# Kernel tuning notes

Hardware: AMD Instinct MI355X
Metric: run time of the kernel (lower is better)

The kernel has to match this reference:

```python
import jax, jax.numpy as jnp
import numpy as np
from jax import lax

GROUPS = 32
EPS = 1e-5
COMMON_STRIDE = 4


def conv3x3(x, w):
    # x: [B,C,H,W], w: [O,I,3,3], stride 1, padding 1 ('SAME'), no bias
    return lax.conv_general_dilated(x, w, (1, 1), 'SAME',
                                    dimension_numbers=('NCHW', 'OIHW', 'NCHW'))


def group_norm(x, scale, bias):
    b, c, h, w = x.shape
    xg = x.reshape(b, GROUPS, c // GROUPS, h, w)
    mean = xg.mean(axis=(2, 3, 4), keepdims=True)
    var = xg.var(axis=(2, 3, 4), keepdims=True)
    xg = (xg - mean) * lax.rsqrt(var + EPS)
    x = xg.reshape(b, c, h, w)
    return x * scale[None, :, None, None] + bias[None, :, None, None]


def head(x, w, s, bta):
    return jax.nn.relu(group_norm(conv3x3(x, w), s, bta))


def setup_inputs() -> dict:
    key = jax.random.key(0)
    ks = jax.random.split(key, 4)
    B, Cin, H, W = 2, 256, 64, 64
    Cd, K = 128, 19
    fan3 = Cin * 9
    return {
        'x': jax.random.normal(ks[0], (B, Cin, H, W), jnp.float32),
        'w_pam': jax.random.normal(ks[1], (Cd, Cin, 3, 3), jnp.float32) * np.sqrt(2.0 / fan3),
        'gn_pam_scale': jnp.ones((Cd,), jnp.float32),
        'gn_pam_bias': jnp.zeros((Cd,), jnp.float32),
        'w_cam': jax.random.normal(ks[2], (Cd, Cin, 3, 3), jnp.float32) * np.sqrt(2.0 / fan3),
        'gn_cam_scale': jnp.ones((Cd,), jnp.float32),
        'gn_cam_bias': jnp.zeros((Cd,), jnp.float32),
        'w_pred': jax.random.normal(ks[3], (K, Cd, 1, 1), jnp.float32) * np.sqrt(2.0 / Cd),
        'b_pred': jnp.zeros((K,), jnp.float32),
    }


def reference(x, w_pam, gn_pam_scale, gn_pam_bias, w_cam, gn_cam_scale, gn_cam_bias,
              w_pred, b_pred):
    pam = head(x, w_pam, gn_pam_scale, gn_pam_bias)   # [B,C,H,W]
    cam = head(x, w_cam, gn_cam_scale, gn_cam_bias)   # [B,C,H,W]
    b, c, h, w = pam.shape
    n = h * w

    # --- PAM: spatial self-attention, unscaled QK^T softmax V (Q=K=V=pam) ---
    Bm = pam.reshape(b, c, n)                                   # [B,C,N]
    pam_w = jax.nn.softmax(jnp.einsum('bci,bcj->bij', Bm, Bm), axis=-1)  # [B,N,N]
    weighted_pam = jnp.einsum('bij,bcj->bci', pam_w, Bm).reshape(b, c, h, w)
    sum_pam = pam + weighted_pam

    # --- CAM: channel self-attention over [C,C] gram matrix ---
    Am = cam.reshape(b, c, n)                                   # [B,C,N]
    cam_w = jax.nn.softmax(jnp.einsum('bcn,bdn->bcd', Am, Am), axis=-1)  # [B,C,C]
    weighted_cam = jnp.einsum('bcd,bdn->bcn', cam_w, Am).reshape(b, c, h, w)
    sum_cam = cam + weighted_cam

    # --- predictor (1x1 conv with bias) + bilinear upsample x common_stride ---
    fused = sum_pam + sum_cam
    logits = jnp.einsum('bchw,kc->bkhw', fused, w_pred[:, :, 0, 0]) + b_pred[None, :, None, None]
    out = jax.image.resize(logits, (b, logits.shape[1], h * COMMON_STRIDE, w * COMMON_STRIDE),
                           method='bilinear')  # half-pixel centers == align_corners=False
    return out
```

## Files before the change

### kernel.cpp

```cpp
#include <hip/hip_runtime.h>

#define BB 2
#define CIN 256
#define HH 64
#define WW 64
#define NPIX 4096
#define CD 128
#define CO2 256
#define KOUT 19
#define EPSV 1e-5f
#define SPAD 4356
#define KW9 2304

typedef __attribute__((ext_vector_type(8))) short bf16x8;
typedef __attribute__((ext_vector_type(4))) float f32x4;

__device__ inline unsigned short f2bf(float f) {
  unsigned u = __float_as_uint(f);
  u += 0x7fffu + ((u >> 16) & 1u);
  return (unsigned short)(u >> 16);
}
__device__ inline float bf2f(unsigned short h) {
  return __uint_as_float((unsigned)h << 16);
}
__device__ inline void f2bf_pair(float f, unsigned short& hi, unsigned short& lo) {
  hi = f2bf(f);
  const float fhi = __uint_as_float((unsigned)hi << 16);
  lo = f2bf(f - fhi);
}

__global__ __launch_bounds__(64) void zhalo_kernel(
    unsigned short* __restrict__ xThi, unsigned short* __restrict__ xTlo)
{
  const int p = blockIdx.x;
  const int b = blockIdx.y;
  int s;
  if (p < 66) s = p;
  else if (p < 132) s = 65 * 66 + (p - 66);
  else { const int q = p - 132; s = (1 + (q >> 1)) * 66 + (q & 1) * 65; }
  const size_t o = ((size_t)b * SPAD + s) * 256 + threadIdx.x * 4;
  *reinterpret_cast<uint2*>(&xThi[o]) = make_uint2(0, 0);
  *reinterpret_cast<uint2*>(&xTlo[o]) = make_uint2(0, 0);
}

__global__ __launch_bounds__(256) void xpose_kernel(
    const float* __restrict__ x, unsigned short* __restrict__ xThi,
    unsigned short* __restrict__ xTlo)
{
  const int y = blockIdx.x;
  const int cig = blockIdx.y;
  const int b = blockIdx.z;
  __shared__ float Tl[32][65];
  const int t = threadIdx.x;
  {
    const int cl = t >> 3, pg = t & 7;
    const float* src = x + ((size_t)(b * CIN + cig * 32 + cl)) * NPIX + y * 64 + pg * 8;
    const float4 v0 = *reinterpret_cast<const float4*>(src);
    const float4 v1 = *reinterpret_cast<const float4*>(src + 4);
    Tl[cl][pg * 8 + 0] = v0.x; Tl[cl][pg * 8 + 1] = v0.y;
    Tl[cl][pg * 8 + 2] = v0.z; Tl[cl][pg * 8 + 3] = v0.w;
    Tl[cl][pg * 8 + 4] = v1.x; Tl[cl][pg * 8 + 5] = v1.y;
    Tl[cl][pg * 8 + 6] = v1.z; Tl[cl][pg * 8 + 7] = v1.w;
  }
  __syncthreads();
  {
    const int sl = t >> 2, cg = t & 3;
    unsigned short hh[8], ll[8];
    #pragma unroll
    for (int i = 0; i < 8; ++i) f2bf_pair(Tl[cg * 8 + i][sl], hh[i], ll[i]);
    uint4 ph, pl;
    ph.x = (unsigned)hh[0] | ((unsigned)hh[1] << 16);
    ph.y = (unsigned)hh[2] | ((unsigned)hh[3] << 16);
    ph.z = (unsigned)hh[4] | ((unsigned)hh[5] << 16);
    ph.w = (unsigned)hh[6] | ((unsigned)hh[7] << 16);
    pl.x = (unsigned)ll[0] | ((unsigned)ll[1] << 16);
    pl.y = (unsigned)ll[2] | ((unsigned)ll[3] << 16);
    pl.z = (unsigned)ll[4] | ((unsigned)ll[5] << 16);
    pl.w = (unsigned)ll[6] | ((unsigned)ll[7] << 16);
    const size_t o = ((size_t)b * SPAD + (y + 1) * 66 + 1 + sl) * 256 + cig * 32 + cg * 8;
    *reinterpret_cast<uint4*>(&xThi[o]) = ph;
    *reinterpret_cast<uint4*>(&xTlo[o]) = pl;
  }
}

__global__ __launch_bounds__(256) void wbconv_kernel(
    const float* __restrict__ w_pam, const float* __restrict__ w_cam,
    unsigned short* __restrict__ wbhi, unsigned short* __restrict__ wblo)
{
  const int co = blockIdx.x;
  const float* wsrc = (co < CD) ? (w_pam + (size_t)co * KW9)
                                : (w_cam + (size_t)(co - CD) * KW9);
  const int t = threadIdx.x;
  #pragma unroll
  for (int i = 0; i < 9; ++i) {
    const int idx = i * 256 + t;
    const int q = idx >> 8, ci = idx & 255;
    unsigned short h, l;
    f2bf_pair(wsrc[ci * 9 + q], h, l);
    const size_t dest = ((((size_t)(co >> 4) * 9 + q) * 8 + (ci >> 5)) * 4
                        + ((ci >> 3) & 3)) * 128 + (co & 15) * 8 + (ci & 7);
    wbhi[dest] = h;
    wblo[dest] = l;
  }
}

__global__ __launch_bounds__(256) void conv_mfma_kernel(
    const unsigned short* __restrict__ xThi, const unsigned short* __restrict__ xTlo,
    const unsigned short* __restrict__ wbhi, const unsigned short* __restrict__ wblo,
    float* __restrict__ out)
{
  const int pxt = blockIdx.x;
  const int cot = blockIdx.y;
  const int b = blockIdx.z;
  const int tid = threadIdx.x;
  const int w = tid >> 6;
  const int lane = tid & 63;
  const int m = lane & 15, g = lane >> 4;
  const int p0 = pxt * 64;
  const int y = p0 >> 6;
  const int sbase = (y + 1) * 66 + 1;

  __shared__ float Obuf[4][64][68];

  const size_t xb = (size_t)b * SPAD * 256;

  f32x4 acc[4][4];
  #pragma unroll
  for (int mt = 0; mt < 4; ++mt)
    #pragma unroll
    for (int jg = 0; jg < 4; ++jg)
      #pragma unroll
      for (int r = 0; r < 4; ++r) acc[mt][jg][r] = 0.f;

  for (int q = 0; q < 9; ++q) {
    const int dq = (q / 3 - 1) * 66 + (q % 3 - 1);
    const unsigned short* xh0 = xThi + xb + (size_t)(sbase + m + dq) * 256;
    const unsigned short* xl0 = xTlo + xb + (size_t)(sbase + m + dq) * 256;
    #pragma unroll
    for (int kk2 = 0; kk2 < 2; ++kk2) {
      const int kkc = w * 2 + kk2;
      const int ko = kkc * 32 + g * 8;
      bf16x8 bh[4], bl[4];
      #pragma unroll
      for (int jg = 0; jg < 4; ++jg) {
        bh[jg] = *reinterpret_cast<const bf16x8*>(&xh0[(size_t)(jg * 16) * 256 + ko]);
        bl[jg] = *reinterpret_cast<const bf16x8*>(&xl0[(size_t)(jg * 16) * 256 + ko]);
      }
      #pragma unroll
      for (int mt = 0; mt < 4; ++mt) {
        const size_t wbase = ((((size_t)(cot * 4 + mt) * 9 + q) * 8 + kkc) * 4 + g) * 128
                             + m * 8;
        const bf16x8 ah = *reinterpret_cast<const bf16x8*>(&wbhi[wbase]);
        const bf16x8 al = *reinterpret_cast<const bf16x8*>(&wblo[wbase]);
        #pragma unroll
        for (int jg = 0; jg < 4; ++jg) {
          acc[mt][jg] = __builtin_amdgcn_mfma_f32_16x16x32_bf16(ah, bh[jg], acc[mt][jg], 0, 0, 0);
          acc[mt][jg] = __builtin_amdgcn_mfma_f32_16x16x32_bf16(ah, bl[jg], acc[mt][jg], 0, 0, 0);
          acc[mt][jg] = __builtin_amdgcn_mfma_f32_16x16x32_bf16(al, bh[jg], acc[mt][jg], 0, 0, 0);
        }
      }
    }
  }

  #pragma unroll
  for (int mt = 0; mt < 4; ++mt)
    #pragma unroll
    for (int jg = 0; jg < 4; ++jg)
      #pragma unroll
      for (int r = 0; r < 4; ++r)
        Obuf[w][mt * 16 + g * 4 + r][jg * 16 + m] = acc[mt][jg][r];
  __syncthreads();

  const int co_l = tid >> 2;
  const int pxq = (tid & 3) * 16;
  float* op = out + ((size_t)b * CO2 + cot * 64 + co_l) * NPIX + p0 + pxq;
  #pragma unroll
  for (int i = 0; i < 4; ++i) {
    float4 s;
    s.x = Obuf[0][co_l][pxq + i * 4 + 0] + Obuf[1][co_l][pxq + i * 4 + 0]
        + Obuf[2][co_l][pxq + i * 4 + 0] + Obuf[3][co_l][pxq + i * 4 + 0];
    s.y = Obuf[0][co_l][pxq + i * 4 + 1] + Obuf[1][co_l][pxq + i * 4 + 1]
        + Obuf[2][co_l][pxq + i * 4 + 1] + Obuf[3][co_l][pxq + i * 4 + 1];
    s.z = Obuf[0][co_l][pxq + i * 4 + 2] + Obuf[1][co_l][pxq + i * 4 + 2]
        + Obuf[2][co_l][pxq + i * 4 + 2] + Obuf[3][co_l][pxq + i * 4 + 2];
    s.w = Obuf[0][co_l][pxq + i * 4 + 3] + Obuf[1][co_l][pxq + i * 4 + 3]
        + Obuf[2][co_l][pxq + i * 4 + 3] + Obuf[3][co_l][pxq + i * 4 + 3];
    *reinterpret_cast<float4*>(&op[i * 4]) = s;
  }
}

__global__ __launch_bounds__(256) void gn_stats_kernel(
    const float* __restrict__ conv, float* __restrict__ meanb, float* __restrict__ rstdb)
{
  const int g = blockIdx.x;
  const float* base = conv + (size_t)g * (4 * NPIX);
  float s = 0.f, ss = 0.f;
  const float4* b4 = reinterpret_cast<const float4*>(base);
  for (int i = threadIdx.x; i < 4096; i += 256) {
    float4 v = b4[i];
    s += v.x + v.y + v.z + v.w;
    ss += v.x * v.x + v.y * v.y + v.z * v.z + v.w * v.w;
  }
  #pragma unroll
  for (int off = 32; off > 0; off >>= 1) {
    s += __shfl_down(s, off);
    ss += __shfl_down(ss, off);
  }
  __shared__ float rs[4], rss[4];
  const int lane = threadIdx.x & 63, wv = threadIdx.x >> 6;
  if (lane == 0) { rs[wv] = s; rss[wv] = ss; }
  __syncthreads();
  if (threadIdx.x == 0) {
    const float S = rs[0] + rs[1] + rs[2] + rs[3];
    const float SS = rss[0] + rss[1] + rss[2] + rss[3];
    const float inv = 1.f / 16384.f;
    const float m = S * inv;
    const float var = SS * inv - m * m;
    meanb[g] = m;
    rstdb[g] = rsqrtf(var + EPSV);
  }
}

__global__ __launch_bounds__(256) void gn_pack_kernel(
    float* __restrict__ conv, const float* __restrict__ meanb, const float* __restrict__ rstdb,
    const float* __restrict__ sc_pam, const float* __restrict__ bi_pam,
    const float* __restrict__ sc_cam, const float* __restrict__ bi_cam,
    unsigned short* __restrict__ Kf2, unsigned short* __restrict__ Vf2)
{
  const int px0 = blockIdx.x * 64;
  const int c0  = blockIdx.y * 32;
  const int b   = blockIdx.z;
  __shared__ unsigned short Tl[32][76];
  const int t = threadIdx.x;
  {
    const int cl = t >> 3, pg = t & 7;
    const int c = c0 + cl;
    const int gi = (b * 256 + c) >> 2;
    const int head = c >> 7, cc = c & 127;
    const float mean = meanb[gi], rstd = rstdb[gi];
    const float sc = head ? sc_cam[cc] : sc_pam[cc];
    const float bi = head ? bi_cam[cc] : bi_pam[cc];
    float* src = conv + ((size_t)b * CO2 + c) * NPIX + px0 + pg * 8;
    float4 v0 = *reinterpret_cast<const float4*>(src);
    float4 v1 = *reinterpret_cast<const float4*>(src + 4);
    v0.x = fmaxf((v0.x - mean) * rstd * sc + bi, 0.f);
    v0.y = fmaxf((v0.y - mean) * rstd * sc + bi, 0.f);
    v0.z = fmaxf((v0.z - mean) * rstd * sc + bi, 0.f);
    v0.w = fmaxf((v0.w - mean) * rstd * sc + bi, 0.f);
    v1.x = fmaxf((v1.x - mean) * rstd * sc + bi, 0.f);
    v1.y = fmaxf((v1.y - mean) * rstd * sc + bi, 0.f);
    v1.z = fmaxf((v1.z - mean) * rstd * sc + bi, 0.f);
    v1.w = fmaxf((v1.w - mean) * rstd * sc + bi, 0.f);
    *reinterpret_cast<float4*>(src) = v0;
    *reinterpret_cast<float4*>(src + 4) = v1;
    Tl[cl][pg * 8 + 0] = f2bf(v0.x); Tl[cl][pg * 8 + 1] = f2bf(v0.y);
    Tl[cl][pg * 8 + 2] = f2bf(v0.z); Tl[cl][pg * 8 + 3] = f2bf(v0.w);
    Tl[cl][pg * 8 + 4] = f2bf(v1.x); Tl[cl][pg * 8 + 5] = f2bf(v1.y);
    Tl[cl][pg * 8 + 6] = f2bf(v1.z); Tl[cl][pg * 8 + 7] = f2bf(v1.w);
  }
  __syncthreads();
  if (c0 < CD) {
    unsigned short* Kb = Kf2 + (size_t)b * 524288;
    unsigned short* Vb = Vf2 + (size_t)b * 524288;
    {
      const int jblk_l = t >> 6, rem = t & 63;
      const int gk = rem >> 4, mk = rem & 15;
      const int jblk = (px0 >> 4) + jblk_l;
      const int kk = c0 >> 5;
      unsigned short h[8];
      #pragma unroll
      for (int e = 0; e < 8; ++e) h[e] = Tl[gk * 8 + e][jblk_l * 16 + mk];
      uint4 packed;
      packed.x = (unsigned)h[0] | ((unsigned)h[1] << 16);
      packed.y = (unsigned)h[2] | ((unsigned)h[3] << 16);
      packed.z = (unsigned)h[4] | ((unsigned)h[5] << 16);
      packed.w = (unsigned)h[6] | ((unsigned)h[7] << 16);
      *reinterpret_cast<uint4*>(&Kb[(size_t)(jblk * 16 + kk * 4 + gk) * 128 + mk * 8]) = packed;
    }
    {
      const int ct_l = t >> 7, kt = (t >> 6) & 1, gv = (t >> 4) & 3, mv = t & 15;
      const int ct = (c0 >> 4) + ct_l;
      const int jc = px0 >> 6;
      unsigned short h[8];
      #pragma unroll
      for (int e = 0; e < 8; ++e) h[e] = Tl[ct_l * 16 + mv][kt * 32 + gv * 8 + e];
      uint4 packed;
      packed.x = (unsigned)h[0] | ((unsigned)h[1] << 16);
      packed.y = (unsigned)h[2] | ((unsigned)h[3] << 16);
      packed.z = (unsigned)h[4] | ((unsigned)h[5] << 16);
      packed.w = (unsigned)h[6] | ((unsigned)h[7] << 16);
      *reinterpret_cast<uint4*>(
          &Vb[(size_t)(((ct * 64 + jc) * 2 + kt) * 4 + gv) * 128 + mv * 8]) = packed;
    }
  }
}

__global__ __launch_bounds__(512) void pam_mfma_kernel(
    const unsigned short* __restrict__ Kf2, const unsigned short* __restrict__ Vf2,
    unsigned short* __restrict__ Opart, float* __restrict__ mpart,
    float* __restrict__ lpart)
{
  const int tile = blockIdx.x;
  const int b = blockIdx.y;
  const int kg = blockIdx.z;
  const int q0 = tile * 32;
  const int tid = threadIdx.x;
  const int w = tid >> 6;
  const int lane = tid & 63;
  const int m = lane & 15, g = lane >> 4;

  __shared__ __align__(16) unsigned short Sl[8][32 * 72];
  __shared__ unsigned short Obuf[4][32][130];
  __shared__ float mlm[8][32], mll[8][32], mst[32], ltt[32];

  const unsigned short* Kb = Kf2 + (size_t)b * 524288;
  const unsigned short* Vb = Vf2 + (size_t)b * 524288;

  bf16x8 qf[2][4];
  #pragma unroll
  for (int s = 0; s < 2; ++s)
    #pragma unroll
    for (int kk = 0; kk < 4; ++kk)
      qf[s][kk] = *reinterpret_cast<const bf16x8*>(
          &Kb[(size_t)(((q0 >> 4) + s) * 16 + kk * 4 + g) * 128 + m * 8]);

  f32x4 oacc[2][8];
  #pragma unroll
  for (int s = 0; s < 2; ++s)
    #pragma unroll
    for (int ct = 0; ct < 8; ++ct)
      #pragma unroll
      for (int r = 0; r < 4; ++r) oacc[s][ct][r] = 0.f;

  float mrow[2][4], lrow[2][4];
  #pragma unroll
  for (int s = 0; s < 2; ++s)
    #pragma unroll
    for (int r = 0; r < 4; ++r) { mrow[s][r] = -1e30f; lrow[s][r] = 0.f; }

  for (int t = kg * 32 + w * 4; t < kg * 32 + w * 4 + 4; ++t) {
    f32x4 sacc[2][4];
    #pragma unroll
    for (int s = 0; s < 2; ++s)
      #pragma unroll
      for (int jt = 0; jt < 4; ++jt)
        #pragma unroll
        for (int r = 0; r < 4; ++r) sacc[s][jt][r] = 0.f;
    #pragma unroll
    for (int jt = 0; jt < 4; ++jt) {
      #pragma unroll
      for (int kk = 0; kk < 4; ++kk) {
        const bf16x8 kf = *reinterpret_cast<const bf16x8*>(
            &Kb[(size_t)((t * 4 + jt) * 16 + kk * 4 + g) * 128 + m * 8]);
        sacc[0][jt] = __builtin_amdgcn_mfma_f32_16x16x32_bf16(qf[0][kk], kf, sacc[0][jt], 0, 0, 0);
        sacc[1][jt] = __builtin_amdgcn_mfma_f32_16x16x32_bf16(qf[1][kk], kf, sacc[1][jt], 0, 0, 0);
      }
    }
    float facq[2];
    #pragma unroll
    for (int s = 0; s < 2; ++s) {
      float fac[4];
      #pragma unroll
      for (int r = 0; r < 4; ++r) {
        float v = fmaxf(fmaxf(sacc[s][0][r], sacc[s][1][r]), fmaxf(sacc[s][2][r], sacc[s][3][r]));
        v = fmaxf(v, __shfl_xor(v, 1));
        v = fmaxf(v, __shfl_xor(v, 2));
        v = fmaxf(v, __shfl_xor(v, 4));
        v = fmaxf(v, __shfl_xor(v, 8));
        const float mn = fmaxf(mrow[s][r], v);
        fac[r] = __expf(fmaxf(mrow[s][r] - mn, -80.f));
        mrow[s][r] = mn;
      }
      #pragma unroll
      for (int r = 0; r < 4; ++r) {
        float ls = 0.f;
        #pragma unroll
        for (int jt = 0; jt < 4; ++jt) {
          const float e = __expf(sacc[s][jt][r] - mrow[s][r]);
          ls += e;
          Sl[w][(s * 16 + g * 4 + r) * 72 + jt * 16 + m] = f2bf(e);
        }
        ls += __shfl_xor(ls, 1);
        ls += __shfl_xor(ls, 2);
        ls += __shfl_xor(ls, 4);
        ls += __shfl_xor(ls, 8);
        lrow[s][r] = lrow[s][r] * fac[r] + ls;
      }
      const int sel = m & 3;
      const float fsel = (sel == 0) ? fac[0] : (sel == 1) ? fac[1] : (sel == 2) ? fac[2] : fac[3];
      facq[s] = __shfl(fsel, ((m >> 2) << 4) | sel);
    }
    #pragma unroll
    for (int s = 0; s < 2; ++s)
      #pragma unroll
      for (int ct = 0; ct < 8; ++ct)
        #pragma unroll
        for (int r = 0; r < 4; ++r) oacc[s][ct][r] *= facq[s];
    bf16x8 pf[2][2];
    #pragma unroll
    for (int s = 0; s < 2; ++s)
      #pragma unroll
      for (int kt = 0; kt < 2; ++kt)
        pf[s][kt] = *reinterpret_cast<const bf16x8*>(&Sl[w][(s * 16 + m) * 72 + kt * 32 + g * 8]);
    #pragma unroll
    for (int ct = 0; ct < 8; ++ct) {
      #pragma unroll
      for (int kt = 0; kt < 2; ++kt) {
        const bf16x8 vf = *reinterpret_cast<const bf16x8*>(
            &Vb[(size_t)(((ct * 64 + t) * 2 + kt) * 4 + g) * 128 + m * 8]);
        oacc[0][ct] = __builtin_amdgcn_mfma_f32_16x16x32_bf16(vf, pf[0][kt], oacc[0][ct], 0, 0, 0);
        oacc[1][ct] = __builtin_amdgcn_mfma_f32_16x16x32_bf16(vf, pf[1][kt], oacc[1][ct], 0, 0, 0);
      }
    }
  }

  float mq[2], lq[2];
  #pragma unroll
  for (int s = 0; s < 2; ++s) {
    const int sel = m & 3;
    const float msel_ = (sel == 0) ? mrow[s][0] : (sel == 1) ? mrow[s][1]
                       : (sel == 2) ? mrow[s][2] : mrow[s][3];
    mq[s] = __shfl(msel_, ((m >> 2) << 4) | sel);
    const float lsel_ = (sel == 0) ? lrow[s][0] : (sel == 1) ? lrow[s][1]
                       : (sel == 2) ? lrow[s][2] : lrow[s][3];
    lq[s] = __shfl(lsel_, ((m >> 2) << 4) | sel);
  }
  if (g == 0) {
    #pragma unroll
    for (int s = 0; s < 2; ++s) { mlm[w][s * 16 + m] = mq[s]; mll[w][s * 16 + m] = lq[s]; }
  }
  __syncthreads();
  float rsw[2];
  #pragma unroll
  for (int s = 0; s < 2; ++s) {
    const int row = s * 16 + m;
    float ms = mlm[0][row];
    #pragma unroll
    for (int sw = 1; sw < 8; ++sw) ms = fmaxf(ms, mlm[sw][row]);
    rsw[s] = __expf(fmaxf(mq[s] - ms, -80.f));
  }
  if (w < 4) {
    #pragma unroll
    for (int s = 0; s < 2; ++s)
      #pragma unroll
      for (int ct = 0; ct < 8; ++ct)
        #pragma unroll
        for (int r = 0; r < 4; ++r)
          Obuf[w][s * 16 + m][ct * 16 + g * 4 + r] = f2bf(oacc[s][ct][r] * rsw[s]);
  }
  if (w == 0 && g == 0) {
    #pragma unroll
    for (int s = 0; s < 2; ++s) {
      const int row = s * 16 + m;
      float ms = mlm[0][row];
      #pragma unroll
      for (int sw = 1; sw < 8; ++sw) ms = fmaxf(ms, mlm[sw][row]);
      float lt = 0.f;
      #pragma unroll
      for (int sw = 0; sw < 8; ++sw)
        lt += mll[sw][row] * __expf(fmaxf(mlm[sw][row] - ms, -80.f));
      mst[row] = ms;
      ltt[row] = lt;
    }
  }
  __syncthreads();
  if (w >= 4) {
    #pragma unroll
    for (int s = 0; s < 2; ++s)
      #pragma unroll
      for (int ct = 0; ct < 8; ++ct)
        #pragma unroll
        for (int r = 0; r < 4; ++r) {
          unsigned short* pp = &Obuf[w - 4][s * 16 + m][ct * 16 + g * 4 + r];
          *pp = f2bf(bf2f(*pp) + oacc[s][ct][r] * rsw[s]);
        }
  }
  __syncthreads();
  const size_t pbase = ((size_t)(kg * BB + b) * 128 + tile) * 32;
  unsigned short* Op = Opart + pbase * 128;
  const int c = tid >> 2;
  const int qh = (tid & 3) * 8;
  #pragma unroll
  for (int qq = 0; qq < 8; ++qq) {
    const int row = qh + qq;
    float o = 0.f;
    #pragma unroll
    for (int sw = 0; sw < 4; ++sw) o += bf2f(Obuf[sw][row][c]);
    Op[(size_t)row * 128 + c] = f2bf(o);
  }
  if (tid < 32) {
    mpart[pbase + tid] = mst[tid];
    lpart[pbase + tid] = ltt[tid];
  }
}

__global__ __launch_bounds__(256) void pam_merge_kernel(
    const float* __restrict__ conv, const unsigned short* __restrict__ Opart,
    const float* __restrict__ mpart, const float* __restrict__ lpart,
    float* __restrict__ spam)
{
  const int tile = blockIdx.x;
  const int b = blockIdx.y;
  const int tid = threadIdx.x;
  const int c = tid & 127;
  const int rg = tid >> 7;
  const size_t i0 = ((size_t)(0 * BB + b) * 128 + tile) * 32;
  const size_t i1 = ((size_t)(1 * BB + b) * 128 + tile) * 32;
  #pragma unroll
  for (int rr = 0; rr < 16; ++rr) {
    const int row = rg * 16 + rr;
    const float m0 = mpart[i0 + row], m1 = mpart[i1 + row];
    const float ms = fmaxf(m0, m1);
    const float w0 = __expf(fmaxf(m0 - ms, -80.f));
    const float w1 = __expf(fmaxf(m1 - ms, -80.f));
    const float l = lpart[i0 + row] * w0 + lpart[i1 + row] * w1;
    const float o = bf2f(Opart[(i0 + row) * 128 + c]) * w0
                  + bf2f(Opart[(i1 + row) * 128 + c]) * w1;
    const int q = tile * 32 + row;
    spam[((size_t)b * CD + c) * NPIX + q] =
        conv[((size_t)b * CO2 + c) * NPIX + q] + o / l;
  }
}

__global__ __launch_bounds__(256) void cam_gram_kernel(
    const float* __restrict__ conv, float* __restrict__ gpart)
{
  const int slice = blockIdx.x;
  const int b = blockIdx.y;
  const float* Am = conv + ((size_t)b * CO2 + CD) * NPIX;
  __shared__ float As[128][65];
  const int tid = threadIdx.x;
  const int cgrp = tid >> 4, dgrp = tid & 15;
  float acc[8][8];
  #pragma unroll
  for (int i = 0; i < 8; ++i)
    #pragma unroll
    for (int j = 0; j < 8; ++j) acc[i][j] = 0.f;
  const int nn = tid & 63, c0 = tid >> 6;
  for (int sub = 0; sub < 2; ++sub) {
    const int n0 = slice * 128 + sub * 64;
    __syncthreads();
    #pragma unroll
    for (int k = 0; k < 32; ++k)
      As[c0 + 4 * k][nn] = Am[(size_t)(c0 + 4 * k) * NPIX + n0 + nn];
    __syncthreads();
    #pragma unroll 4
    for (int n = 0; n < 64; ++n) {
      float av[8], bv[8];
      #pragma unroll
      for (int i = 0; i < 8; ++i) av[i] = As[8 * cgrp + i][n];
      #pragma unroll
      for (int j = 0; j < 8; ++j) bv[j] = As[8 * dgrp + j][n];
      #pragma unroll
      for (int i = 0; i < 8; ++i)
        #pragma unroll
        for (int j = 0; j < 8; ++j)
          acc[i][j] += av[i] * bv[j];
    }
  }
  float* gp = gpart + (((size_t)slice * BB + b) * CD + 8 * cgrp) * CD + 8 * dgrp;
  #pragma unroll
  for (int i = 0; i < 8; ++i)
    #pragma unroll
    for (int j = 0; j < 8; ++j)
      gp[i * CD + j] = acc[i][j];
}

__global__ __launch_bounds__(128) void cam_softmax_kernel(
    const float* __restrict__ gpart, float* __restrict__ camw)
{
  const int bc = blockIdx.x;
  const int b = bc >> 7, c = bc & 127;
  const int d = threadIdx.x;
  float g = 0.f;
  for (int s = 0; s < 32; ++s)
    g += gpart[(((size_t)s * BB + b) * CD + c) * CD + d];
  float m = g;
  #pragma unroll
  for (int off = 32; off > 0; off >>= 1) m = fmaxf(m, __shfl_xor(m, off));
  __shared__ float sm[2], ssum[2];
  const int lane = d & 63, wv = d >> 6;
  if (lane == 0) sm[wv] = m;
  __syncthreads();
  m = fmaxf(sm[0], sm[1]);
  const float e = __expf(g - m);
  float s = e;
  #pragma unroll
  for (int off = 32; off > 0; off >>= 1) s += __shfl_xor(s, off);
  if (lane == 0) ssum[wv] = s;
  __syncthreads();
  camw[(size_t)bc * CD + d] = e / (ssum[0] + ssum[1]);
}

__global__ __launch_bounds__(256) void cam_apply_kernel(
    const float* __restrict__ conv, const float* __restrict__ camw, float* __restrict__ scam)
{
  const int b = blockIdx.z;
  const int c0 = blockIdx.y * 4;
  const int n = blockIdx.x * 1024 + threadIdx.x;
  const float* Am = conv + ((size_t)b * CO2 + CD) * NPIX;
  const float* Wr = camw + ((size_t)b * CD + c0) * CD;
  float acc[4][4];
  #pragma unroll
  for (int i = 0; i < 4; ++i)
    #pragma unroll
    for (int k = 0; k < 4; ++k) acc[i][k] = 0.f;
  for (int d = 0; d < CD; ++d) {
    const float w0 = Wr[d], w1 = Wr[CD + d], w2 = Wr[2 * CD + d], w3 = Wr[3 * CD + d];
    #pragma unroll
    for (int k = 0; k < 4; ++k) {
      const float a = Am[(size_t)d * NPIX + n + k * 256];
      acc[0][k] += w0 * a; acc[1][k] += w1 * a;
      acc[2][k] += w2 * a; acc[3][k] += w3 * a;
    }
  }
  #pragma unroll
  for (int i = 0; i < 4; ++i)
    #pragma unroll
    for (int k = 0; k < 4; ++k)
      scam[((size_t)b * CD + c0 + i) * NPIX + n + k * 256] =
          Am[(size_t)(c0 + i) * NPIX + n + k * 256] + acc[i][k];
}

__global__ __launch_bounds__(256) void pred_part_kernel(
    const float* __restrict__ spam, const float* __restrict__ scam,
    const float* __restrict__ wpred, float* __restrict__ psum)
{
  const int p = blockIdx.x * 256 + threadIdx.x;
  const int slice = blockIdx.y;
  const int b = blockIdx.z;
  float acc[KOUT];
  #pragma unroll
  for (int k = 0; k < KOUT; ++k) acc[k] = 0.f;
  const float* sp = spam + (size_t)b * CD * NPIX + p;
  const float* sc = scam + (size_t)b * CD * NPIX + p;
  #pragma unroll
  for (int ci = 0; ci < 16; ++ci) {
    const int c = slice * 16 + ci;
    const float f = sp[(size_t)c * NPIX] + sc[(size_t)c * NPIX];
    #pragma unroll
    for (int k = 0; k < KOUT; ++k)
      acc[k] += f * wpred[k * CD + c];
  }
  #pragma unroll
  for (int k = 0; k < KOUT; ++k)
    psum[(((size_t)slice * BB + b) * KOUT + k) * NPIX + p] = acc[k];
}

__global__ __launch_bounds__(256) void pred_reduce_kernel(
    const float* __restrict__ psum, const float* __restrict__ bpred,
    float* __restrict__ logit)
{
  const int p = blockIdx.x * 256 + threadIdx.x;
  const int b = blockIdx.y;
  #pragma unroll
  for (int k = 0; k < KOUT; ++k) {
    float s = bpred[k];
    #pragma unroll
    for (int sl = 0; sl < 8; ++sl)
      s += psum[(((size_t)sl * BB + b) * KOUT + k) * NPIX + p];
    logit[((size_t)b * KOUT + k) * NPIX + p] = s;
  }
}

__global__ __launch_bounds__(256) void upsample_kernel(
    const float* __restrict__ logit, float* __restrict__ out)
{
  const int idx = blockIdx.x * 256 + threadIdx.x;
  if (idx >= BB * KOUT * 256 * 256) return;
  const int ox = idx & 255;
  const int oy = (idx >> 8) & 255;
  const int plane = idx >> 16;
  const float* src = logit + (size_t)plane * NPIX;
  const float sy = (oy + 0.5f) * 0.25f - 0.5f;
  const float sx = (ox + 0.5f) * 0.25f - 0.5f;
  const float fyf = floorf(sy), fxf = floorf(sx);
  const float wy = sy - fyf, wx = sx - fxf;
  const int y0 = (int)fyf, x0 = (int)fxf;
  const int y0c = y0 < 0 ? 0 : y0;
  const int y1c = (y0 + 1 > 63) ? 63 : y0 + 1;
  const int x0c = x0 < 0 ? 0 : x0;
  const int x1c = (x0 + 1 > 63) ? 63 : x0 + 1;
  const float v00 = src[y0c * 64 + x0c], v01 = src[y0c * 64 + x1c];
  const float v10 = src[y1c * 64 + x0c], v11 = src[y1c * 64 + x1c];
  const float top = v00 + (v01 - v00) * wx;
  const float bot = v10 + (v11 - v10) * wx;
  out[idx] = top + (bot - top) * wy;
}

extern "C" void kernel_launch(void* const* d_in, const int* in_sizes, int n_in,
                              void* d_out, int out_size, void* d_ws, size_t ws_size,
                              hipStream_t stream) {
  (void)in_sizes; (void)n_in; (void)out_size; (void)ws_size;
  const float* x      = (const float*)d_in[0];
  const float* w_pam  = (const float*)d_in[1];
  const float* s_pam  = (const float*)d_in[2];
  const float* b_pam  = (const float*)d_in[3];
  const float* w_cam  = (const float*)d_in[4];
  const float* s_cam  = (const float*)d_in[5];
  const float* b_cam  = (const float*)d_in[6];
  const float* w_pred = (const float*)d_in[7];
  const float* b_pred = (const float*)d_in[8];
  float* out_f = (float*)d_out;
  float* ws0 = (float*)d_ws;

  float* conv  = ws0;
  unsigned short* xThi = (unsigned short*)(ws0 + 2097152);
  unsigned short* xTlo = xThi + (size_t)BB * SPAD * 256;
  unsigned short* wbhi = (unsigned short*)(ws0 + 4327424);
  unsigned short* wblo = wbhi + (size_t)CO2 * KW9;
  float* gpart = ws0 + 3145728;
  unsigned short* Opart = (unsigned short*)(ws0 + 3145728);
  float* mpart = ws0 + 4194304;
  float* lpart = ws0 + 4227072;
  float* psum  = ws0 + 3145728;
  float* camw  = ws0 + 4950016;
  float* meanb = ws0 + 4982784;
  float* rstdb = ws0 + 4982912;
  float* logit = ws0 + 4983040;

  unsigned short* Kf2 = xThi;
  unsigned short* Vf2 = Kf2 + 1048576;

  float* spam = out_f;
  float* scam = out_f + 1048576;

  zhalo_kernel<<<dim3(260, 2), 64, 0, stream>>>(xThi, xTlo);
  xpose_kernel<<<dim3(64, 8, 2), 256, 0, stream>>>(x, xThi, xTlo);
  wbconv_kernel<<<256, 256, 0, stream>>>(w_pam, w_cam, wbhi, wblo);
  conv_mfma_kernel<<<dim3(64, 4, 2), 256, 0, stream>>>(xThi, xTlo, wbhi, wblo, conv);
  gn_stats_kernel<<<128, 256, 0, stream>>>(conv, meanb, rstdb);
  gn_pack_kernel<<<dim3(64, 8, 2), 256, 0, stream>>>(conv, meanb, rstdb,
      s_pam, b_pam, s_cam, b_cam, Kf2, Vf2);
  cam_gram_kernel<<<dim3(32, 2), 256, 0, stream>>>(conv, gpart);
  cam_softmax_kernel<<<256, 128, 0, stream>>>(gpart, camw);
  cam_apply_kernel<<<dim3(4, 32, 2), 256, 0, stream>>>(conv, camw, scam);
  pam_mfma_kernel<<<dim3(128, 2, 2), 512, 0, stream>>>(Kf2, Vf2, Opart, mpart, lpart);
  pam_merge_kernel<<<dim3(128, 2), 256, 0, stream>>>(conv, Opart, mpart, lpart, spam);
  pred_part_kernel<<<dim3(16, 8, 2), 256, 0, stream>>>(spam, scam, w_pred, psum);
  pred_reduce_kernel<<<dim3(16, 2), 256, 0, stream>>>(psum, b_pred, logit);
  upsample_kernel<<<9728, 256, 0, stream>>>(logit, out_f);
}
```

Measured before the change: 247.9 us.

## Compute CAM gram matrix with split-bf16 MFMA from packed fragments

The CAM channel gram matrix now runs on bf16 MFMA instructions instead of an FP32 SIMT outer-product kernel. gn_pack writes the CAM activations as hi/lo bf16 pairs in an MFMA fragment layout, and three MFMAs per tile approximate FP32 accuracy. The new gram kernel reduces over waves in shared memory and writes the final gram directly, so the softmax no longer sums 32 partial slices. The trade-off is extra pack work and hi/lo storage, and the gram launches only 16 blocks, which may leave most compute units idle.

```diff
diff --git a/kernel.cpp b/kernel.cpp
--- a/kernel.cpp
+++ b/kernel.cpp
@@ -225,12 +225,13 @@
     float* __restrict__ conv, const float* __restrict__ meanb, const float* __restrict__ rstdb,
     const float* __restrict__ sc_pam, const float* __restrict__ bi_pam,
     const float* __restrict__ sc_cam, const float* __restrict__ bi_cam,
-    unsigned short* __restrict__ Kf2, unsigned short* __restrict__ Vf2)
+    unsigned short* __restrict__ Kf2, unsigned short* __restrict__ Vf2,
+    unsigned short* __restrict__ Cfhi, unsigned short* __restrict__ Cflo)
 {
   const int px0 = blockIdx.x * 64;
   const int c0  = blockIdx.y * 32;
   const int b   = blockIdx.z;
-  __shared__ unsigned short Tl[32][76];
+  __shared__ float Tl[32][72];
   const int t = threadIdx.x;
   {
     const int cl = t >> 3, pg = t & 7;
@@ -253,10 +254,10 @@
     v1.w = fmaxf((v1.w - mean) * rstd * sc + bi, 0.f);
     *reinterpret_cast<float4*>(src) = v0;
     *reinterpret_cast<float4*>(src + 4) = v1;
-    Tl[cl][pg * 8 + 0] = f2bf(v0.x); Tl[cl][pg * 8 + 1] = f2bf(v0.y);
-    Tl[cl][pg * 8 + 2] = f2bf(v0.z); Tl[cl][pg * 8 + 3] = f2bf(v0.w);
-    Tl[cl][pg * 8 + 4] = f2bf(v1.x); Tl[cl][pg * 8 + 5] = f2bf(v1.y);
-    Tl[cl][pg * 8 + 6] = f2bf(v1.z); Tl[cl][pg * 8 + 7] = f2bf(v1.w);
+    Tl[cl][pg * 8 + 0] = v0.x; Tl[cl][pg * 8 + 1] = v0.y;
+    Tl[cl][pg * 8 + 2] = v0.z; Tl[cl][pg * 8 + 3] = v0.w;
+    Tl[cl][pg * 8 + 4] = v1.x; Tl[cl][pg * 8 + 5] = v1.y;
+    Tl[cl][pg * 8 + 6] = v1.z; Tl[cl][pg * 8 + 7] = v1.w;
   }
   __syncthreads();
   if (c0 < CD) {
@@ -269,7 +270,7 @@
       const int kk = c0 >> 5;
       unsigned short h[8];
       #pragma unroll
-      for (int e = 0; e < 8; ++e) h[e] = Tl[gk * 8 + e][jblk_l * 16 + mk];
+      for (int e = 0; e < 8; ++e) h[e] = f2bf(Tl[gk * 8 + e][jblk_l * 16 + mk]);
       uint4 packed;
       packed.x = (unsigned)h[0] | ((unsigned)h[1] << 16);
       packed.y = (unsigned)h[2] | ((unsigned)h[3] << 16);
@@ -283,7 +284,7 @@
       const int jc = px0 >> 6;
       unsigned short h[8];
       #pragma unroll
-      for (int e = 0; e < 8; ++e) h[e] = Tl[ct_l * 16 + mv][kt * 32 + gv * 8 + e];
+      for (int e = 0; e < 8; ++e) h[e] = f2bf(Tl[ct_l * 16 + mv][kt * 32 + gv * 8 + e]);
       uint4 packed;
       packed.x = (unsigned)h[0] | ((unsigned)h[1] << 16);
       packed.y = (unsigned)h[2] | ((unsigned)h[3] << 16);
@@ -292,7 +293,139 @@
       *reinterpret_cast<uint4*>(
           &Vb[(size_t)(((ct * 64 + jc) * 2 + kt) * 4 + gv) * 128 + mv * 8]) = packed;
     }
-  }
+  } else {
+    const int ct_l = t >> 7, kk_l = (t >> 6) & 1, gc = (t >> 4) & 3, mc = t & 15;
+    const int ctg = ((c0 - CD) >> 4) + ct_l;
+    const int kkg = (px0 >> 5) + kk_l;
+    unsigned short hh[8], ll[8];
+    #pragma unroll
+    for (int e = 0; e < 8; ++e)
+      f2bf_pair(Tl[ct_l * 16 + mc][kk_l * 32 + gc * 8 + e], hh[e], ll[e]);
+    uint4 ph, pl;
+    ph.x = (unsigned)hh[0] | ((unsigned)hh[1] << 16);
+    ph.y = (unsigned)hh[2] | ((unsigned)hh[3] << 16);
+    ph.z = (unsigned)hh[4] | ((unsigned)hh[5] << 16);
+    ph.w = (unsigned)hh[6] | ((unsigned)hh[7] << 16);
+    pl.x = (unsigned)ll[0] | ((unsigned)ll[1] << 16);
+    pl.y = (unsigned)ll[2] | ((unsigned)ll[3] << 16);
+    pl.z = (unsigned)ll[4] | ((unsigned)ll[5] << 16);
+    pl.w = (unsigned)ll[6] | ((unsigned)ll[7] << 16);
+    const size_t o = (((size_t)(b * 128 + kkg) * 8 + ctg) * 4 + gc) * 128 + mc * 8;
+    *reinterpret_cast<uint4*>(&Cfhi[o]) = ph;
+    *reinterpret_cast<uint4*>(&Cflo[o]) = pl;
+  }
+}
+
+__global__ __launch_bounds__(512) void cam_gram_mfma_kernel(
+    const unsigned short* __restrict__ Cfhi, const unsigned short* __restrict__ Cflo,
+    float* __restrict__ graw)
+{
+  const int dt = blockIdx.x;
+  const int b = blockIdx.y;
+  const int tid = threadIdx.x;
+  const int w = tid >> 6;
+  const int lane = tid & 63;
+  const int m = lane & 15, g = lane >> 4;
+
+  __shared__ float Gbuf[4][128][17];
+
+  f32x4 acc[8];
+  #pragma unroll
+  for (int ct = 0; ct < 8; ++ct)
+    #pragma unroll
+    for (int r = 0; r < 4; ++r) acc[ct][r] = 0.f;
+
+  for (int kk = w * 16; kk < w * 16 + 16; ++kk) {
+    const size_t base = (size_t)(b * 128 + kk) * 8;
+    const bf16x8 dh = *reinterpret_cast<const bf16x8*>(&Cfhi[((base + dt) * 4 + g) * 128 + m * 8]);
+    const bf16x8 dl = *reinterpret_cast<const bf16x8*>(&Cflo[((base + dt) * 4 + g) * 128 + m * 8]);
+    #pragma unroll
+    for (int ct = 0; ct < 8; ++ct) {
+      const bf16x8 ah = *reinterpret_cast<const bf16x8*>(&Cfhi[((base + ct) * 4 + g) * 128 + m * 8]);
+      const bf16x8 al = *reinterpret_cast<const bf16x8*>(&Cflo[((base + ct) * 4 + g) * 128 + m * 8]);
+      acc[ct] = __builtin_amdgcn_mfma_f32_16x16x32_bf16(ah, dh, acc[ct], 0, 0, 0);
+      acc[ct] = __builtin_amdgcn_mfma_f32_16x16x32_bf16(ah, dl, acc[ct], 0, 0, 0);
+      acc[ct] = __builtin_amdgcn_mfma_f32_16x16x32_bf16(al, dh, acc[ct], 0, 0, 0);
+    }
+  }
+
+  if (w < 4) {
+    #pragma unroll
+    for (int ct = 0; ct < 8; ++ct)
+      #pragma unroll
+      for (int r = 0; r < 4; ++r)
+        Gbuf[w][ct * 16 + g * 4 + r][m] = acc[ct][r];
+  }
+  __syncthreads();
+  if (w >= 4) {
+    #pragma unroll
+    for (int ct = 0; ct < 8; ++ct)
+      #pragma unroll
+      for (int r = 0; r < 4; ++r)
+        Gbuf[w - 4][ct * 16 + g * 4 + r][m] += acc[ct][r];
+  }
+  __syncthreads();
+  const int c = tid >> 2;
+  const int d0 = (tid & 3) * 4;
+  #pragma unroll
+  for (int j = 0; j < 4; ++j) {
+    const int d = d0 + j;
+    graw[((size_t)(b * 128 + c)) * 128 + dt * 16 + d] =
+        Gbuf[0][c][d] + Gbuf[1][c][d] + Gbuf[2][c][d] + Gbuf[3][c][d];
+  }
+}
+
+__global__ __launch_bounds__(128) void cam_softmax_kernel(
+    const float* __restrict__ graw, float* __restrict__ camw)
+{
+  const int bc = blockIdx.x;
+  const int d = threadIdx.x;
+  const float g = graw[(size_t)bc * CD + d];
+  float m = g;
+  #pragma unroll
+  for (int off = 32; off > 0; off >>= 1) m = fmaxf(m, __shfl_xor(m, off));
+  __shared__ float sm[2], ssum[2];
+  const int lane = d & 63, wv = d >> 6;
+  if (lane == 0) sm[wv] = m;
+  __syncthreads();
+  m = fmaxf(sm[0], sm[1]);
+  const float e = __expf(g - m);
+  float s = e;
+  #pragma unroll
+  for (int off = 32; off > 0; off >>= 1) s += __shfl_xor(s, off);
+  if (lane == 0) ssum[wv] = s;
+  __syncthreads();
+  camw[(size_t)bc * CD + d] = e / (ssum[0] + ssum[1]);
+}
+
+__global__ __launch_bounds__(256) void cam_apply_kernel(
+    const float* __restrict__ conv, const float* __restrict__ camw, float* __restrict__ scam)
+{
+  const int b = blockIdx.z;
+  const int c0 = blockIdx.y * 4;
+  const int n = blockIdx.x * 1024 + threadIdx.x;
+  const float* Am = conv + ((size_t)b * CO2 + CD) * NPIX;
+  const float* Wr = camw + ((size_t)b * CD + c0) * CD;
+  float acc[4][4];
+  #pragma unroll
+  for (int i = 0; i < 4; ++i)
+    #pragma unroll
+    for (int k = 0; k < 4; ++k) acc[i][k] = 0.f;
+  for (int d = 0; d < CD; ++d) {
+    const float w0 = Wr[d], w1 = Wr[CD + d], w2 = Wr[2 * CD + d], w3 = Wr[3 * CD + d];
+    #pragma unroll
+    for (int k = 0; k < 4; ++k) {
+      const float a = Am[(size_t)d * NPIX + n + k * 256];
+      acc[0][k] += w0 * a; acc[1][k] += w1 * a;
+      acc[2][k] += w2 * a; acc[3][k] += w3 * a;
+    }
+  }
+  #pragma unroll
+  for (int i = 0; i < 4; ++i)
+    #pragma unroll
+    for (int k = 0; k < 4; ++k)
+      scam[((size_t)b * CD + c0 + i) * NPIX + n + k * 256] =
+          Am[(size_t)(c0 + i) * NPIX + n + k * 256] + acc[i][k];
 }
 
 __global__ __launch_bounds__(512) void pam_mfma_kernel(
@@ -520,106 +653,6 @@
     spam[((size_t)b * CD + c) * NPIX + q] =
         conv[((size_t)b * CO2 + c) * NPIX + q] + o / l;
   }
-}
-
-__global__ __launch_bounds__(256) void cam_gram_kernel(
-    const float* __restrict__ conv, float* __restrict__ gpart)
-{
-  const int slice = blockIdx.x;
-  const int b = blockIdx.y;
-  const float* Am = conv + ((size_t)b * CO2 + CD) * NPIX;
-  __shared__ float As[128][65];
-  const int tid = threadIdx.x;
-  const int cgrp = tid >> 4, dgrp = tid & 15;
-  float acc[8][8];
-  #pragma unroll
-  for (int i = 0; i < 8; ++i)
-    #pragma unroll
-    for (int j = 0; j < 8; ++j) acc[i][j] = 0.f;
-  const int nn = tid & 63, c0 = tid >> 6;
-  for (int sub = 0; sub < 2; ++sub) {
-    const int n0 = slice * 128 + sub * 64;
-    __syncthreads();
-    #pragma unroll
-    for (int k = 0; k < 32; ++k)
-      As[c0 + 4 * k][nn] = Am[(size_t)(c0 + 4 * k) * NPIX + n0 + nn];
-    __syncthreads();
-    #pragma unroll 4
-    for (int n = 0; n < 64; ++n) {
-      float av[8], bv[8];
-      #pragma unroll
-      for (int i = 0; i < 8; ++i) av[i] = As[8 * cgrp + i][n];
-      #pragma unroll
-      for (int j = 0; j < 8; ++j) bv[j] = As[8 * dgrp + j][n];
-      #pragma unroll
-      for (int i = 0; i < 8; ++i)
-        #pragma unroll
-        for (int j = 0; j < 8; ++j)
-          acc[i][j] += av[i] * bv[j];
-    }
-  }
-  float* gp = gpart + (((size_t)slice * BB + b) * CD + 8 * cgrp) * CD + 8 * dgrp;
-  #pragma unroll
-  for (int i = 0; i < 8; ++i)
-    #pragma unroll
-    for (int j = 0; j < 8; ++j)
-      gp[i * CD + j] = acc[i][j];
-}
-
-__global__ __launch_bounds__(128) void cam_softmax_kernel(
-    const float* __restrict__ gpart, float* __restrict__ camw)
-{
-  const int bc = blockIdx.x;
-  const int b = bc >> 7, c = bc & 127;
-  const int d = threadIdx.x;
-  float g = 0.f;
-  for (int s = 0; s < 32; ++s)
-    g += gpart[(((size_t)s * BB + b) * CD + c) * CD + d];
-  float m = g;
-  #pragma unroll
-  for (int off = 32; off > 0; off >>= 1) m = fmaxf(m, __shfl_xor(m, off));
-  __shared__ float sm[2], ssum[2];
-  const int lane = d & 63, wv = d >> 6;
-  if (lane == 0) sm[wv] = m;
-  __syncthreads();
-  m = fmaxf(sm[0], sm[1]);
-  const float e = __expf(g - m);
-  float s = e;
-  #pragma unroll
-  for (int off = 32; off > 0; off >>= 1) s += __shfl_xor(s, off);
-  if (lane == 0) ssum[wv] = s;
-  __syncthreads();
-  camw[(size_t)bc * CD + d] = e / (ssum[0] + ssum[1]);
-}
-
-__global__ __launch_bounds__(256) void cam_apply_kernel(
-    const float* __restrict__ conv, const float* __restrict__ camw, float* __restrict__ scam)
-{
-  const int b = blockIdx.z;
-  const int c0 = blockIdx.y * 4;
-  const int n = blockIdx.x * 1024 + threadIdx.x;
-  const float* Am = conv + ((size_t)b * CO2 + CD) * NPIX;
-  const float* Wr = camw + ((size_t)b * CD + c0) * CD;
-  float acc[4][4];
-  #pragma unroll
-  for (int i = 0; i < 4; ++i)
-    #pragma unroll
-    for (int k = 0; k < 4; ++k) acc[i][k] = 0.f;
-  for (int d = 0; d < CD; ++d) {
-    const float w0 = Wr[d], w1 = Wr[CD + d], w2 = Wr[2 * CD + d], w3 = Wr[3 * CD + d];
-    #pragma unroll
-    for (int k = 0; k < 4; ++k) {
-      const float a = Am[(size_t)d * NPIX + n + k * 256];
-      acc[0][k] += w0 * a; acc[1][k] += w1 * a;
-      acc[2][k] += w2 * a; acc[3][k] += w3 * a;
-    }
-  }
-  #pragma unroll
-  for (int i = 0; i < 4; ++i)
-    #pragma unroll
-    for (int k = 0; k < 4; ++k)
-      scam[((size_t)b * CD + c0 + i) * NPIX + n + k * 256] =
-          Am[(size_t)(c0 + i) * NPIX + n + k * 256] + acc[i][k];
 }
 
 __global__ __launch_bounds__(256) void pred_part_kernel(
@@ -709,11 +742,13 @@
   unsigned short* xTlo = xThi + (size_t)BB * SPAD * 256;
   unsigned short* wbhi = (unsigned short*)(ws0 + 4327424);
   unsigned short* wblo = wbhi + (size_t)CO2 * KW9;
-  float* gpart = ws0 + 3145728;
+  unsigned short* Cfhi = (unsigned short*)(ws0 + 3145728);
+  unsigned short* Cflo = (unsigned short*)(ws0 + 3670016);
   unsigned short* Opart = (unsigned short*)(ws0 + 3145728);
+  float* psum  = ws0 + 3145728;
   float* mpart = ws0 + 4194304;
   float* lpart = ws0 + 4227072;
-  float* psum  = ws0 + 3145728;
+  float* graw  = ws0 + 4259840;
   float* camw  = ws0 + 4950016;
   float* meanb = ws0 + 4982784;
   float* rstdb = ws0 + 4982912;
@@ -731,9 +766,9 @@
   conv_mfma_kernel<<<dim3(64, 4, 2), 256, 0, stream>>>(xThi, xTlo, wbhi, wblo, conv);
   gn_stats_kernel<<<128, 256, 0, stream>>>(conv, meanb, rstdb);
   gn_pack_kernel<<<dim3(64, 8, 2), 256, 0, stream>>>(conv, meanb, rstdb,
-      s_pam, b_pam, s_cam, b_cam, Kf2, Vf2);
-  cam_gram_kernel<<<dim3(32, 2), 256, 0, stream>>>(conv, gpart);
-  cam_softmax_kernel<<<256, 128, 0, stream>>>(gpart, camw);
+      s_pam, b_pam, s_cam, b_cam, Kf2, Vf2, Cfhi, Cflo);
+  cam_gram_mfma_kernel<<<dim3(8, 2), 512, 0, stream>>>(Cfhi, Cflo, graw);
+  cam_softmax_kernel<<<256, 128, 0, stream>>>(graw, camw);
   cam_apply_kernel<<<dim3(4, 32, 2), 256, 0, stream>>>(conv, camw, scam);
   pam_mfma_kernel<<<dim3(128, 2, 2), 512, 0, stream>>>(Kf2, Vf2, Opart, mpart, lpart);
   pam_merge_kernel<<<dim3(128, 2), 256, 0, stream>>>(conv, Opart, mpart, lpart, spam);
```

Result: slower. 278.9 us (+12.5%).
